# Optimization experiments

Measured on AMD Instinct MI355X. Metric: run time of the kernel, lower is better.

## Reference

```python
import jax, jax.numpy as jnp
import numpy as np

NUM_HEADS = 16
HIDDEN = 1024
TOTAL = 2048
NSEG = 8


def setup_inputs() -> dict:
    key = jax.random.key(0)
    ks = jax.random.split(key, 10)
    x = jax.random.normal(ks[0], (TOTAL, HIDDEN), dtype=jnp.float32)
    # cu_seqlens: [0, b1, ..., TOTAL], sorted segment boundaries
    inner = np.sort(np.random.default_rng(0).integers(1, TOTAL, size=NSEG - 1))
    cu_seqlens = jnp.asarray(np.concatenate([[0], inner, [TOTAL]]), dtype=jnp.int32)
    s = 1.0 / np.sqrt(HIDDEN)
    def lin(k):
        kw, kb = jax.random.split(k)
        W = jax.random.uniform(kw, (HIDDEN, HIDDEN), jnp.float32, -s, s)
        b = jax.random.uniform(kb, (HIDDEN,), jnp.float32, -s, s)
        return W, b
    Wq, bq = lin(ks[1]); Wk, bk = lin(ks[2]); Wv, bv = lin(ks[3]); Wo, bo = lin(ks[4])
    return {"hidden_states_packed": x, "cu_seqlens": cu_seqlens,
            "Wq": Wq, "bq": bq, "Wk": Wk, "bk": bk,
            "Wv": Wv, "bv": bv, "Wo": Wo, "bo": bo}


def reference(hidden_states_packed, cu_seqlens, Wq, bq, Wk, bk, Wv, bv, Wo, bo):
    T, H = hidden_states_packed.shape
    dh = H // NUM_HEADS
    x = hidden_states_packed
    q = (x @ Wq.T + bq).reshape(T, NUM_HEADS, dh)
    k = (x @ Wk.T + bk).reshape(T, NUM_HEADS, dh)
    v = (x @ Wv.T + bv).reshape(T, NUM_HEADS, dh)
    # segment id of each token from cu_seqlens boundaries
    seg = jnp.searchsorted(cu_seqlens, jnp.arange(T, dtype=jnp.int32), side="right")
    same_seg = seg[:, None] == seg[None, :]  # [T, T] block-diagonal mask
    scale = 1.0 / jnp.sqrt(jnp.asarray(dh, x.dtype))
    scores = jnp.einsum("qhd,khd->hqk", q, k) * scale  # [H, T, T]
    neg = jnp.asarray(jnp.finfo(scores.dtype).min, scores.dtype)
    scores = jnp.where(same_seg[None, :, :], scores, neg)
    attn = jax.nn.softmax(scores, axis=-1)
    ctx = jnp.einsum("hqk,khd->qhd", attn, v).reshape(T, H)
    return ctx @ Wo.T + bo
```

## Files before the change

kernel.cpp:

```cpp
#include <hip/hip_runtime.h>

typedef _Float16 f16x8 __attribute__((ext_vector_type(8)));
typedef _Float16 f16x4 __attribute__((ext_vector_type(4)));
typedef float    f32x4 __attribute__((ext_vector_type(4)));

#define MFMA_F16(a, b, c) __builtin_amdgcn_mfma_f32_16x16x32_f16((a), (b), (c), 0, 0, 0)

typedef __attribute__((address_space(1))) void gas_void;
typedef __attribute__((address_space(3))) void las_void;
#define GLOAD_LDS16(g, l) \
  __builtin_amdgcn_global_load_lds((gas_void*)(g), (las_void*)(l), 16, 0, 0)

#define NEG_INF (-__builtin_inff())

constexpr int T_SEQ  = 2048;
constexpr int HID    = 1024;
constexpr int NHEADS = 16;
constexpr int DH     = 64;
constexpr int NSEG   = 8;

__global__ __launch_bounds__(256) void convert_all(
    const float* __restrict__ x,
    const float* __restrict__ Wq, const float* __restrict__ Wk,
    const float* __restrict__ Wv, const float* __restrict__ Wo,
    _Float16* __restrict__ xh,
    _Float16* __restrict__ Wqh, _Float16* __restrict__ Wkh,
    _Float16* __restrict__ Wvh, _Float16* __restrict__ Woh) {
  int i = blockIdx.x * 256 + threadIdx.x;
  const float* src;
  _Float16* dst;
  int local;
  if (i < 524288) {
    src = x; dst = xh; local = i;
  } else {
    int j = i - 524288;
    int w = j >> 18;
    local = j & 262143;
    src = (w == 0) ? Wq : (w == 1) ? Wk : (w == 2) ? Wv : Wo;
    dst = (w == 0) ? Wqh : (w == 1) ? Wkh : (w == 2) ? Wvh : Woh;
  }
  float4 f = *(const float4*)(src + (size_t)local * 4);
  f16x4 h;
  h[0] = (_Float16)f.x; h[1] = (_Float16)f.y;
  h[2] = (_Float16)f.z; h[3] = (_Float16)f.w;
  *(f16x4*)(dst + (size_t)local * 4) = h;
}

template <int LAYOUT, int BM, int BN>
__device__ __forceinline__ void gemm_t(const _Float16* __restrict__ A,
                                       const _Float16* __restrict__ B,
                                       const float* __restrict__ bias,
                                       _Float16* __restrict__ outh,
                                       float* __restrict__ outf) {
  constexpr int K = HID, N = HID;
  constexpr int MI = BM / 32;
  constexpr int NI = BN / 32;
  constexpr int LA = (BM * 64) / (256 * 8);
  constexpr int LB = (BN * 64) / (256 * 8);
  __shared__ _Float16 As[BM * 64];
  __shared__ _Float16 Bs[BN * 64];
  const int tid  = threadIdx.x;
  const int wave = tid >> 6, lane = tid & 63;
  const int lr = lane & 15, lq = lane >> 4;
  const int wm = (wave >> 1) * (BM / 2);
  const int wn = (wave & 1) * (BN / 2);
  const int bm = blockIdx.y * BM, bn = blockIdx.x * BN;

  const _Float16* gA[LA];
  const _Float16* gB[LB];
  _Float16* lA[LA];
  _Float16* lB[LB];
#pragma unroll
  for (int i = 0; i < LA; ++i) {
    const int s = i * 256 + tid;
    const int row = s >> 3, pch = s & 7;
    const int lch = pch ^ (row & 7);
    gA[i] = A + (size_t)(bm + row) * K + lch * 8;
    lA[i] = &As[(i * 256 + wave * 64) * 8];
  }
#pragma unroll
  for (int i = 0; i < LB; ++i) {
    const int s = i * 256 + tid;
    const int row = s >> 3, pch = s & 7;
    const int lch = pch ^ (row & 7);
    gB[i] = B + (size_t)(bn + row) * K + lch * 8;
    lB[i] = &Bs[(i * 256 + wave * 64) * 8];
  }

  f32x4 acc[MI][NI] = {};

  for (int kk = 0; kk < K; kk += 64) {
#pragma unroll
    for (int i = 0; i < LA; ++i) GLOAD_LDS16(gA[i] + kk, lA[i]);
#pragma unroll
    for (int i = 0; i < LB; ++i) GLOAD_LDS16(gB[i] + kk, lB[i]);
    __syncthreads();
#pragma unroll
    for (int ks = 0; ks < 2; ++ks) {
      f16x8 af[MI], bf[NI];
#pragma unroll
      for (int mi = 0; mi < MI; ++mi) {
        const int row = wm + mi * 16 + lr;
        af[mi] = *(const f16x8*)&As[row * 64 + (((ks * 4 + lq) ^ (row & 7)) * 8)];
      }
#pragma unroll
      for (int ni = 0; ni < NI; ++ni) {
        const int row = wn + ni * 16 + lr;
        bf[ni] = *(const f16x8*)&Bs[row * 64 + (((ks * 4 + lq) ^ (row & 7)) * 8)];
      }
#pragma unroll
      for (int mi = 0; mi < MI; ++mi)
#pragma unroll
        for (int ni = 0; ni < NI; ++ni)
          acc[mi][ni] = MFMA_F16(af[mi], bf[ni], acc[mi][ni]);
    }
    __syncthreads();
  }

#pragma unroll
  for (int ni = 0; ni < NI; ++ni) {
    const int col = bn + wn + ni * 16 + lr;
    const float bv = bias[col];
#pragma unroll
    for (int mi = 0; mi < MI; ++mi) {
      const f32x4 v = acc[mi][ni];
      const int row0 = bm + wm + mi * 16 + lq * 4;
      if (LAYOUT == 3) {
        f16x4 o;
#pragma unroll
        for (int r = 0; r < 4; ++r) o[r] = (_Float16)(v[r] + bv);
        *(f16x4*)&outh[(size_t)col * T_SEQ + row0] = o;
      } else {
#pragma unroll
        for (int r = 0; r < 4; ++r) {
          const int row = row0 + r;
          const float val = v[r] + bv;
          if (LAYOUT == 0)
            outh[((size_t)(col >> 6) * T_SEQ + row) * DH + (col & 63)] = (_Float16)val;
          else
            outf[(size_t)row * N + col] = val;
        }
      }
    }
  }
}

__global__ __launch_bounds__(256) void gemm_qkv(
    const _Float16* __restrict__ xh,
    const _Float16* __restrict__ Wqh, const _Float16* __restrict__ Wkh,
    const _Float16* __restrict__ Wvh,
    const float* __restrict__ bq, const float* __restrict__ bk,
    const float* __restrict__ bv,
    _Float16* __restrict__ qp, _Float16* __restrict__ kp,
    _Float16* __restrict__ vT) {
  const int z = blockIdx.z;
  if (z == 0) {
    gemm_t<0, 64, 128>(xh, Wqh, bq, qp, nullptr);
  } else if (z == 1) {
    gemm_t<0, 64, 128>(xh, Wkh, bk, kp, nullptr);
  } else {
    gemm_t<3, 64, 128>(xh, Wvh, bv, vT, nullptr);
  }
}

__global__ __launch_bounds__(256) void gemm_out(
    const _Float16* __restrict__ ctxh, const _Float16* __restrict__ Woh,
    const float* __restrict__ bo, float* __restrict__ out) {
  gemm_t<1, 64, 64>(ctxh, Woh, bo, nullptr, out);
}

__device__ __forceinline__ float redsum16(float v) {
  v += __shfl_xor(v, 1);
  v += __shfl_xor(v, 2);
  v += __shfl_xor(v, 4);
  v += __shfl_xor(v, 8);
  return v;
}

__global__ __launch_bounds__(512, 4) void attn_kernel(
    const _Float16* __restrict__ qp, const _Float16* __restrict__ kp,
    const _Float16* __restrict__ vT, const int* __restrict__ cu,
    _Float16* __restrict__ ctx) {
  constexpr float SCL2E = 0.125f * 1.44269504f;
  constexpr int PSTR = 72;
  __shared__ _Float16 Ks[2][64 * 64];
  __shared__ _Float16 Vs[2][64 * 64];
  __shared__ _Float16 Pl[8][16 * PSTR];
  float* mO = (float*)&Ks[0][0];
  float* mL = (float*)&Vs[0][0];
  const int h  = blockIdx.x & 15;
  const int q0 = (blockIdx.x >> 4) * 64;
  const int tid = threadIdx.x, wave = tid >> 6, lane = tid & 63;
  const int lr = lane & 15, lq = lane >> 4;
  const int qsub = wave & 3, khalf = wave >> 2;
  const int qw = q0 + qsub * 16;

  int cs[NSEG + 1];
#pragma unroll
  for (int i = 0; i <= NSEG; ++i) cs[i] = cu[i];

  int sstart[4], send[4];
#pragma unroll
  for (int r = 0; r < 4; ++r) {
    const int row = qw + lq * 4 + r;
    sstart[r] = 0; send[r] = T_SEQ;
#pragma unroll
    for (int s = 0; s < NSEG; ++s)
      if (row >= cs[s] && row < cs[s + 1]) { sstart[r] = cs[s]; send[r] = cs[s + 1]; }
  }
  int wlo = 0, whi = T_SEQ, wlo2 = 0;
#pragma unroll
  for (int s = 0; s < NSEG; ++s) {
    if (qw >= cs[s] && qw < cs[s + 1]) { wlo = cs[s]; whi = cs[s + 1]; }
    if (qw + 15 >= cs[s] && qw + 15 < cs[s + 1]) wlo2 = cs[s];
  }
  const bool wsame = (wlo == wlo2);
  int klo = 0, khi = T_SEQ;
#pragma unroll
  for (int s = 0; s < NSEG; ++s) {
    if (q0 >= cs[s] && q0 < cs[s + 1]) klo = cs[s];
    if (q0 + 63 >= cs[s] && q0 + 63 < cs[s + 1]) khi = cs[s + 1];
  }
  klo &= ~63;
  const int range  = khi - klo;
  const int hlen   = ((range + 127) >> 7) << 6;
  const int nsteps = hlen >> 6;
  const int kstart = klo + khalf * hlen;

  const _Float16* qbase = qp + ((size_t)h * T_SEQ + qw + lr) * DH;
  f16x8 qf0 = *(const f16x8*)(qbase + lq * 8);
  f16x8 qf1 = *(const f16x8*)(qbase + 32 + lq * 8);
#pragma unroll
  for (int i = 0; i < 8; ++i) {
    qf0[i] = qf0[i] * (_Float16)SCL2E;
    qf1[i] = qf1[i] * (_Float16)SCL2E;
  }

  const _Float16* kb = kp + (size_t)h * T_SEQ * DH;
  const _Float16* vb = vT + (size_t)h * DH * T_SEQ;

  const int ht = qsub * 64 + lane;
  int kRow[2], kCol[2], vRow[2], vCol[2];
  _Float16* lK[2];
  _Float16* lV[2];
#pragma unroll
  for (int i = 0; i < 2; ++i) {
    const int s = i * 256 + ht;
    const int row = s >> 3, pch = s & 7;
    const int lch = pch ^ (row & 7);
    kRow[i] = row; kCol[i] = lch * 8;
    vRow[i] = row; vCol[i] = lch * 8;
    lK[i] = &Ks[khalf][(i * 256 + qsub * 64) * 8];
    lV[i] = &Vs[khalf][(i * 256 + qsub * 64) * 8];
  }

  float lst[4] = {0.f, 0.f, 0.f, 0.f};
  f32x4 oacc[4];
#pragma unroll
  for (int c = 0; c < 4; ++c) oacc[c] = f32x4{0.f, 0.f, 0.f, 0.f};

  _Float16* pw = &Pl[wave][0];

  for (int s = 0; s < nsteps; ++s) {
    const int kt = kstart + s * 64;
#pragma unroll
    for (int i = 0; i < 2; ++i) {
      const int grow = min(kt + kRow[i], T_SEQ - 1);
      GLOAD_LDS16(kb + (size_t)grow * DH + kCol[i], lK[i]);
    }
#pragma unroll
    for (int i = 0; i < 2; ++i) {
      const int gcol = min(kt + vCol[i], T_SEQ - 8);
      GLOAD_LDS16(vb + (size_t)vRow[i] * T_SEQ + gcol, lV[i]);
    }
    __syncthreads();

    f32x4 sc[4];
#pragma unroll
    for (int n = 0; n < 4; ++n) {
      const int row = n * 16 + lr;
      const f16x8 kf0 =
          *(const f16x8*)&Ks[khalf][row * 64 + (((0 * 4 + lq) ^ (row & 7)) * 8)];
      const f16x8 kf1 =
          *(const f16x8*)&Ks[khalf][row * 64 + (((1 * 4 + lq) ^ (row & 7)) * 8)];
      sc[n] = f32x4{0.f, 0.f, 0.f, 0.f};
      sc[n] = MFMA_F16(qf0, kf0, sc[n]);
      sc[n] = MFMA_F16(qf1, kf1, sc[n]);
    }
    const bool fastTile = wsame && (kt >= wlo) && (kt + 64 <= whi);
    if (fastTile) {
#pragma unroll
      for (int r = 0; r < 4; ++r) {
        float p[4];
#pragma unroll
        for (int n = 0; n < 4; ++n) p[n] = exp2f(sc[n][r]);
        lst[r] += (p[0] + p[1]) + (p[2] + p[3]);
        _Float16* pr = &pw[(lq * 4 + r) * PSTR + lr];
        pr[0]  = (_Float16)p[0];
        pr[16] = (_Float16)p[1];
        pr[32] = (_Float16)p[2];
        pr[48] = (_Float16)p[3];
      }
    } else {
#pragma unroll
      for (int r = 0; r < 4; ++r) {
        float p[4];
#pragma unroll
        for (int n = 0; n < 4; ++n) {
          const int col = kt + n * 16 + lr;
          const float vv =
              (col >= sstart[r] && col < send[r]) ? sc[n][r] : NEG_INF;
          p[n] = exp2f(vv);
        }
        lst[r] += (p[0] + p[1]) + (p[2] + p[3]);
        _Float16* pr = &pw[(lq * 4 + r) * PSTR + lr];
        pr[0]  = (_Float16)p[0];
        pr[16] = (_Float16)p[1];
        pr[32] = (_Float16)p[2];
        pr[48] = (_Float16)p[3];
      }
    }
    const f16x8 pf0 = *(const f16x8*)&pw[lr * PSTR + lq * 8];
    const f16x8 pf1 = *(const f16x8*)&pw[lr * PSTR + 32 + lq * 8];
#pragma unroll
    for (int c = 0; c < 4; ++c) {
      const int row = c * 16 + lr;
      const f16x8 vf0 =
          *(const f16x8*)&Vs[khalf][row * 64 + (((0 * 4 + lq) ^ (row & 7)) * 8)];
      const f16x8 vf1 =
          *(const f16x8*)&Vs[khalf][row * 64 + (((1 * 4 + lq) ^ (row & 7)) * 8)];
      oacc[c] = MFMA_F16(pf0, vf0, oacc[c]);
      oacc[c] = MFMA_F16(pf1, vf1, oacc[c]);
    }
    __syncthreads();
  }

#pragma unroll
  for (int r = 0; r < 4; ++r) lst[r] = redsum16(lst[r]);

  if (khalf) {
#pragma unroll
    for (int c = 0; c < 4; ++c)
#pragma unroll
      for (int r = 0; r < 4; ++r)
        mO[((qsub * 16) + lq * 4 + r) * 64 + c * 16 + lr] = oacc[c][r];
    if (lr == 0) {
#pragma unroll
      for (int r = 0; r < 4; ++r) mL[qsub * 16 + lq * 4 + r] = lst[r];
    }
  }
  __syncthreads();
  if (!khalf) {
#pragma unroll
    for (int r = 0; r < 4; ++r) lst[r] += mL[qsub * 16 + lq * 4 + r];
#pragma unroll
    for (int c = 0; c < 4; ++c)
#pragma unroll
      for (int r = 0; r < 4; ++r) {
        const int row = qw + lq * 4 + r;
        const float val =
            (oacc[c][r] + mO[((qsub * 16) + lq * 4 + r) * 64 + c * 16 + lr]) /
            lst[r];
        ctx[(size_t)row * HID + h * DH + c * 16 + lr] = (_Float16)val;
      }
  }
}

extern "C" void kernel_launch(void* const* d_in, const int* in_sizes, int n_in,
                              void* d_out, int out_size, void* d_ws, size_t ws_size,
                              hipStream_t stream) {
  const float* x  = (const float*)d_in[0];
  const int* cu   = (const int*)d_in[1];
  const float* Wq = (const float*)d_in[2]; const float* bq = (const float*)d_in[3];
  const float* Wk = (const float*)d_in[4]; const float* bk = (const float*)d_in[5];
  const float* Wv = (const float*)d_in[6]; const float* bv = (const float*)d_in[7];
  const float* Wo = (const float*)d_in[8]; const float* bo = (const float*)d_in[9];
  float* out = (float*)d_out;

  char* ws = (char*)d_ws;
  _Float16* xh   = (_Float16*)(ws + (size_t)0);
  _Float16* Wqh  = (_Float16*)(ws + ((size_t)4 << 20));
  _Float16* Wkh  = (_Float16*)(ws + ((size_t)6 << 20));
  _Float16* Wvh  = (_Float16*)(ws + ((size_t)8 << 20));
  _Float16* Woh  = (_Float16*)(ws + ((size_t)10 << 20));
  _Float16* qp   = (_Float16*)(ws + ((size_t)12 << 20));
  _Float16* kp   = (_Float16*)(ws + ((size_t)16 << 20));
  _Float16* vT   = (_Float16*)(ws + ((size_t)20 << 20));
  _Float16* ctxh = (_Float16*)(ws + ((size_t)24 << 20));

  convert_all<<<6144, 256, 0, stream>>>(x, Wq, Wk, Wv, Wo, xh, Wqh, Wkh, Wvh, Woh);
  gemm_qkv<<<dim3(8, 32, 3), 256, 0, stream>>>(xh, Wqh, Wkh, Wvh, bq, bk, bv, qp, kp, vT);
  attn_kernel<<<512, 512, 0, stream>>>(qp, kp, vT, cu, ctxh);
  gemm_out<<<dim3(16, 32), 256, 0, stream>>>(ctxh, Woh, bo, out);
}
```

Before: 135.4 us.

## Fuse fp32-to-fp16 conversion into GEMM tile loads, drop convert kernel

```diff
diff --git a/kernel.cpp b/kernel.cpp
--- a/kernel.cpp
+++ b/kernel.cpp
@@ -19,44 +19,17 @@
 constexpr int DH     = 64;
 constexpr int NSEG   = 8;
 
-__global__ __launch_bounds__(256) void convert_all(
-    const float* __restrict__ x,
-    const float* __restrict__ Wq, const float* __restrict__ Wk,
-    const float* __restrict__ Wv, const float* __restrict__ Wo,
-    _Float16* __restrict__ xh,
-    _Float16* __restrict__ Wqh, _Float16* __restrict__ Wkh,
-    _Float16* __restrict__ Wvh, _Float16* __restrict__ Woh) {
-  int i = blockIdx.x * 256 + threadIdx.x;
-  const float* src;
-  _Float16* dst;
-  int local;
-  if (i < 524288) {
-    src = x; dst = xh; local = i;
-  } else {
-    int j = i - 524288;
-    int w = j >> 18;
-    local = j & 262143;
-    src = (w == 0) ? Wq : (w == 1) ? Wk : (w == 2) ? Wv : Wo;
-    dst = (w == 0) ? Wqh : (w == 1) ? Wkh : (w == 2) ? Wvh : Woh;
-  }
-  float4 f = *(const float4*)(src + (size_t)local * 4);
-  f16x4 h;
-  h[0] = (_Float16)f.x; h[1] = (_Float16)f.y;
-  h[2] = (_Float16)f.z; h[3] = (_Float16)f.w;
-  *(f16x4*)(dst + (size_t)local * 4) = h;
-}
-
-template <int LAYOUT, int BM, int BN>
-__device__ __forceinline__ void gemm_t(const _Float16* __restrict__ A,
-                                       const _Float16* __restrict__ B,
+template <int LAYOUT, int BM, int BN, bool AF16>
+__device__ __forceinline__ void gemm_t(const void* __restrict__ Ap,
+                                       const float* __restrict__ B32,
                                        const float* __restrict__ bias,
                                        _Float16* __restrict__ outh,
                                        float* __restrict__ outf) {
   constexpr int K = HID, N = HID;
   constexpr int MI = BM / 32;
   constexpr int NI = BN / 32;
-  constexpr int LA = (BM * 64) / (256 * 8);
-  constexpr int LB = (BN * 64) / (256 * 8);
+  constexpr int PA = (BM * 64) / (256 * 8);
+  constexpr int PB = (BN * 64) / (256 * 8);
   __shared__ _Float16 As[BM * 64];
   __shared__ _Float16 Bs[BN * 64];
   const int tid  = threadIdx.x;
@@ -66,34 +39,75 @@
   const int wn = (wave & 1) * (BN / 2);
   const int bm = blockIdx.y * BM, bn = blockIdx.x * BN;
 
-  const _Float16* gA[LA];
-  const _Float16* gB[LB];
-  _Float16* lA[LA];
-  _Float16* lB[LB];
-#pragma unroll
-  for (int i = 0; i < LA; ++i) {
+  const _Float16* gA16[PA];
+  _Float16* lA[PA];
+  const float* gA32[PA];
+  _Float16* sA[PA];
+#pragma unroll
+  for (int i = 0; i < PA; ++i) {
     const int s = i * 256 + tid;
     const int row = s >> 3, pch = s & 7;
     const int lch = pch ^ (row & 7);
-    gA[i] = A + (size_t)(bm + row) * K + lch * 8;
-    lA[i] = &As[(i * 256 + wave * 64) * 8];
-  }
-#pragma unroll
-  for (int i = 0; i < LB; ++i) {
+    if (AF16) {
+      gA16[i] = (const _Float16*)Ap + (size_t)(bm + row) * K + lch * 8;
+      lA[i] = &As[(i * 256 + wave * 64) * 8];
+    } else {
+      gA32[i] = (const float*)Ap + (size_t)(bm + row) * K + lch * 8;
+      sA[i] = &As[(size_t)s * 8];
+    }
+  }
+  const float* gB32[PB];
+  _Float16* sB[PB];
+#pragma unroll
+  for (int i = 0; i < PB; ++i) {
     const int s = i * 256 + tid;
     const int row = s >> 3, pch = s & 7;
     const int lch = pch ^ (row & 7);
-    gB[i] = B + (size_t)(bn + row) * K + lch * 8;
-    lB[i] = &Bs[(i * 256 + wave * 64) * 8];
+    gB32[i] = B32 + (size_t)(bn + row) * K + lch * 8;
+    sB[i] = &Bs[(size_t)s * 8];
   }
 
   f32x4 acc[MI][NI] = {};
 
   for (int kk = 0; kk < K; kk += 64) {
-#pragma unroll
-    for (int i = 0; i < LA; ++i) GLOAD_LDS16(gA[i] + kk, lA[i]);
-#pragma unroll
-    for (int i = 0; i < LB; ++i) GLOAD_LDS16(gB[i] + kk, lB[i]);
+    if (AF16) {
+#pragma unroll
+      for (int i = 0; i < PA; ++i) GLOAD_LDS16(gA16[i] + kk, lA[i]);
+    }
+    float4 a0[PA], a1[PA];
+    if (!AF16) {
+#pragma unroll
+      for (int i = 0; i < PA; ++i) {
+        a0[i] = *(const float4*)(gA32[i] + kk);
+        a1[i] = *(const float4*)(gA32[i] + kk + 4);
+      }
+    }
+    float4 b0[PB], b1[PB];
+#pragma unroll
+    for (int i = 0; i < PB; ++i) {
+      b0[i] = *(const float4*)(gB32[i] + kk);
+      b1[i] = *(const float4*)(gB32[i] + kk + 4);
+    }
+    if (!AF16) {
+#pragma unroll
+      for (int i = 0; i < PA; ++i) {
+        f16x8 h;
+        h[0] = (_Float16)a0[i].x; h[1] = (_Float16)a0[i].y;
+        h[2] = (_Float16)a0[i].z; h[3] = (_Float16)a0[i].w;
+        h[4] = (_Float16)a1[i].x; h[5] = (_Float16)a1[i].y;
+        h[6] = (_Float16)a1[i].z; h[7] = (_Float16)a1[i].w;
+        *(f16x8*)sA[i] = h;
+      }
+    }
+#pragma unroll
+    for (int i = 0; i < PB; ++i) {
+      f16x8 h;
+      h[0] = (_Float16)b0[i].x; h[1] = (_Float16)b0[i].y;
+      h[2] = (_Float16)b0[i].z; h[3] = (_Float16)b0[i].w;
+      h[4] = (_Float16)b1[i].x; h[5] = (_Float16)b1[i].y;
+      h[6] = (_Float16)b1[i].z; h[7] = (_Float16)b1[i].w;
+      *(f16x8*)sB[i] = h;
+    }
     __syncthreads();
 #pragma unroll
     for (int ks = 0; ks < 2; ++ks) {
@@ -145,28 +159,28 @@
   }
 }
 
-__global__ __launch_bounds__(256) void gemm_qkv(
-    const _Float16* __restrict__ xh,
-    const _Float16* __restrict__ Wqh, const _Float16* __restrict__ Wkh,
-    const _Float16* __restrict__ Wvh,
+__global__ __launch_bounds__(256, 3) void gemm_qkv(
+    const float* __restrict__ x,
+    const float* __restrict__ Wq, const float* __restrict__ Wk,
+    const float* __restrict__ Wv,
     const float* __restrict__ bq, const float* __restrict__ bk,
     const float* __restrict__ bv,
     _Float16* __restrict__ qp, _Float16* __restrict__ kp,
     _Float16* __restrict__ vT) {
   const int z = blockIdx.z;
   if (z == 0) {
-    gemm_t<0, 64, 128>(xh, Wqh, bq, qp, nullptr);
+    gemm_t<0, 64, 128, false>(x, Wq, bq, qp, nullptr);
   } else if (z == 1) {
-    gemm_t<0, 64, 128>(xh, Wkh, bk, kp, nullptr);
+    gemm_t<0, 64, 128, false>(x, Wk, bk, kp, nullptr);
   } else {
-    gemm_t<3, 64, 128>(xh, Wvh, bv, vT, nullptr);
-  }
-}
-
-__global__ __launch_bounds__(256) void gemm_out(
-    const _Float16* __restrict__ ctxh, const _Float16* __restrict__ Woh,
+    gemm_t<3, 64, 128, false>(x, Wv, bv, vT, nullptr);
+  }
+}
+
+__global__ __launch_bounds__(256, 2) void gemm_out(
+    const _Float16* __restrict__ ctxh, const float* __restrict__ Wo,
     const float* __restrict__ bo, float* __restrict__ out) {
-  gemm_t<1, 64, 64>(ctxh, Woh, bo, nullptr, out);
+  gemm_t<1, 64, 64, true>(ctxh, Wo, bo, nullptr, out);
 }
 
 __device__ __forceinline__ float redsum16(float v) {
@@ -378,18 +392,12 @@
   float* out = (float*)d_out;
 
   char* ws = (char*)d_ws;
-  _Float16* xh   = (_Float16*)(ws + (size_t)0);
-  _Float16* Wqh  = (_Float16*)(ws + ((size_t)4 << 20));
-  _Float16* Wkh  = (_Float16*)(ws + ((size_t)6 << 20));
-  _Float16* Wvh  = (_Float16*)(ws + ((size_t)8 << 20));
-  _Float16* Woh  = (_Float16*)(ws + ((size_t)10 << 20));
-  _Float16* qp   = (_Float16*)(ws + ((size_t)12 << 20));
-  _Float16* kp   = (_Float16*)(ws + ((size_t)16 << 20));
-  _Float16* vT   = (_Float16*)(ws + ((size_t)20 << 20));
-  _Float16* ctxh = (_Float16*)(ws + ((size_t)24 << 20));
-
-  convert_all<<<6144, 256, 0, stream>>>(x, Wq, Wk, Wv, Wo, xh, Wqh, Wkh, Wvh, Woh);
-  gemm_qkv<<<dim3(8, 32, 3), 256, 0, stream>>>(xh, Wqh, Wkh, Wvh, bq, bk, bv, qp, kp, vT);
+  _Float16* qp   = (_Float16*)(ws + (size_t)0);
+  _Float16* kp   = (_Float16*)(ws + ((size_t)4 << 20));
+  _Float16* vT   = (_Float16*)(ws + ((size_t)8 << 20));
+  _Float16* ctxh = (_Float16*)(ws + ((size_t)12 << 20));
+
+  gemm_qkv<<<dim3(8, 32, 3), 256, 0, stream>>>(x, Wq, Wk, Wv, bq, bk, bv, qp, kp, vT);
   attn_kernel<<<512, 512, 0, stream>>>(qp, kp, vT, cu, ctxh);
-  gemm_out<<<dim3(16, 32), 256, 0, stream>>>(ctxh, Woh, bo, out);
-}
+  gemm_out<<<dim3(16, 32), 256, 0, stream>>>(ctxh, Wo, bo, out);
+}
```

Measured after the change: 153.1 us. 13.1% more time.
